# Kernel optimization log

Hardware: AMD Instinct MI355X
Metric: run time of the kernel (lower is better)

The kernel has to match this reference:

```python
import jax, jax.numpy as jnp
import numpy as np

N_CB = 10          # n_codebooks
K = 2048           # codebook_size
D = 256            # codebook_dim
SEM = 256          # semantic_proj_dim
W2V = 1024         # w2v_bert_dim
COMMIT = 0.25      # commitment_cost


def setup_inputs() -> dict:
    key = jax.random.key(0)
    ks = jax.random.split(key, 7)
    B, T = 16, 1024
    z = jax.random.normal(ks[0], (B, T, D), jnp.float32)
    w2v_targets = jax.random.normal(ks[1], (B, T, W2V), jnp.float32)
    # codebooks: uniform(-1/K, 1/K) as in nn.init.uniform_
    E = jax.random.uniform(ks[2], (N_CB, K, D), jnp.float32, -1.0 / K, 1.0 / K)
    # semantic head: Linear(D, SEM) -> GELU -> Linear(SEM, W2V)
    W1 = jax.random.normal(ks[3], (D, SEM), jnp.float32) * (1.0 / np.sqrt(D))
    b1 = jnp.zeros((SEM,), jnp.float32)
    W2 = jax.random.normal(ks[4], (SEM, W2V), jnp.float32) * (1.0 / np.sqrt(SEM))
    b2 = jnp.zeros((W2V,), jnp.float32)
    return {"z": z, "w2v_targets": w2v_targets, "E": E,
            "W1": W1, "b1": b1, "W2": W2, "b2": b2}


def _vq_step(residual, Ei):
    """Single-codebook VQ with straight-through estimator.
    residual: (B,T,D); Ei: (K,D). Returns (z_q, indices, loss)."""
    sg = jax.lax.stop_gradient
    B, T, d = residual.shape
    flat = residual.reshape(-1, d)                      # (N, D)
    dist = (jnp.sum(flat * flat, axis=1, keepdims=True)
            - 2.0 * flat @ Ei.T
            + jnp.sum(Ei * Ei, axis=1))
    idx = jnp.argmin(dist, axis=1).reshape(B, T)        # (B, T)
    q = Ei[idx]                                         # (B, T, D) gather
    commitment_loss = jnp.mean((sg(q) - residual) ** 2)
    embedding_loss = jnp.mean((q - sg(residual)) ** 2)
    loss = embedding_loss + COMMIT * commitment_loss
    z_q = residual + sg(q - residual)                   # straight-through
    return z_q, idx, loss


def reference(z, w2v_targets, E, W1, b1, W2, b2):
    residual = z
    z_q_total = jnp.zeros_like(z)
    codes = []
    vq_loss = jnp.float32(0.0)
    semantic_loss = jnp.float32(0.0)
    for i in range(N_CB):
        z_q_i, idx_i, loss_i = _vq_step(residual, E[i])
        if i == 0:
            # semantic head on CB1 output (torch GELU default = exact erf)
            h = jax.nn.gelu(z_q_i @ W1 + b1, approximate=False)
            predicted = h @ W2 + b2                     # (B, T, W2V)
            semantic_loss = jnp.mean((predicted - w2v_targets) ** 2)
        z_q_total = z_q_total + z_q_i
        residual = residual - jax.lax.stop_gradient(z_q_i)
        vq_loss = vq_loss + loss_i
        codes.append(idx_i)
    all_codes = jnp.stack(codes, axis=-1)               # (B, T, N_CB)
    return z_q_total, all_codes, vq_loss, semantic_loss
```

## Files before the change

kernel.cpp:

```cpp
#include <hip/hip_runtime.h>
#include <float.h>
#include <math.h>

#define NTOK 16384
#define KCB  2048
#define DDIM 256
#define NCB  10
#define MARGIN 1.0e-3f

typedef __attribute__((ext_vector_type(8))) short  short8;
typedef __attribute__((ext_vector_type(4))) float  f32x4;

static __device__ __forceinline__ unsigned short f2bf(float f) {
    unsigned int b = __float_as_uint(f);
    unsigned int r = b + 0x7FFFu + ((b >> 16) & 1u);
    return (unsigned short)(r >> 16);
}
static __device__ __forceinline__ float bf2f(unsigned short h) {
    return __uint_as_float((unsigned int)h << 16);
}

__global__ __launch_bounds__(256) void norms_all_kernel(const float* __restrict__ E,
                                                        const float* __restrict__ z,
                                                        float* __restrict__ sseE,
                                                        float* __restrict__ normA) {
    const int gw   = (blockIdx.x * 256 + threadIdx.x) >> 6;
    const int lane = threadIdx.x & 63;
    const int row  = gw * 4 + (lane >> 4);
    const int l    = lane & 15;
    const float* src = nullptr; float* dst = nullptr;
    if (row < NCB * KCB)             { src = E + (size_t)row * DDIM;               dst = sseE + row; }
    else if (row < NCB * KCB + NTOK) { src = z + (size_t)(row - NCB * KCB) * DDIM; dst = normA + (row - NCB * KCB); }
    float r = 0.f;
    if (src) {
        const float* a = src + ((l >> 3) << 7) + (l & 7);
        float v = a[0];
        r = __fmul_rn(v, v);
        #pragma unroll
        for (int k = 1; k < 16; ++k) { v = a[k * 8]; r = __fadd_rn(r, __fmul_rn(v, v)); }
    }
    r = __fadd_rn(r, __shfl_xor(r, 1, 64));
    r = __fadd_rn(r, __shfl_xor(r, 2, 64));
    r = __fadd_rn(r, __shfl_xor(r, 4, 64));
    r = __fadd_rn(r, __shfl_xor(r, 8, 64));
    if (src && l == 0) *dst = r;
}

__global__ __launch_bounds__(256) void conv_all_kernel(const float* __restrict__ E,
                                                       const float* __restrict__ z,
                                                       const float* __restrict__ W1,
                                                       const float* __restrict__ W2,
                                                       unsigned short* __restrict__ Eh,
                                                       unsigned short* __restrict__ resH,
                                                       unsigned short* __restrict__ w1t,
                                                       unsigned short* __restrict__ w2t) {
    int i = blockIdx.x * 256 + threadIdx.x;
    if (i < 5242880) {
        Eh[i] = f2bf(E[i]);
    } else if (i < 9437184) {
        int j = i - 5242880;
        resH[j] = f2bf(z[j]);
    } else if (i < 9502720) {
        int j = i - 9437184;
        int n = j >> 8, k = j & 255;
        w1t[j] = f2bf(W1[k * 256 + n]);
    } else {
        int j = i - 9502720;
        int n = j >> 8, k = j & 255;
        w2t[j] = f2bf(W2[k * 1024 + n]);
    }
}

__global__ __launch_bounds__(256) void vq_screen(const unsigned short* __restrict__ resH,
                                                 const unsigned short* __restrict__ Ehi,
                                                 const float* __restrict__ sseEi,
                                                 int2* __restrict__ gSlots,
                                                 int* __restrict__ gCnt,
                                                 float* __restrict__ gMin) {
    __shared__ unsigned short sAh[128 * 40];
    __shared__ unsigned short sBh[128 * 40];
    __shared__ float sC[128];
    __shared__ int   lCnt[128];
    __shared__ int2  lSlot[128][4];
    const int tid = threadIdx.x;
    const int wv = tid >> 6, lane = tid & 63;
    const int l15 = lane & 15, qd = lane >> 4;
    const int tile = blockIdx.x >> 4, slice = blockIdx.x & 15;
    const int t0 = tile * 128, c0 = slice * 128;

    if (tid < 128) { lCnt[tid] = 0; sC[tid] = sseEi[c0 + tid]; }
    {
        int2 inf; inf.x = 0x7F800000; inf.y = 0;
        ((int2*)lSlot)[tid] = inf; ((int2*)lSlot)[tid + 256] = inf;
    }

    f32x4 acc[2][8];
    #pragma unroll
    for (int m = 0; m < 2; ++m)
        #pragma unroll
        for (int n = 0; n < 8; ++n) acc[m][n] = (f32x4){0.f, 0.f, 0.f, 0.f};

    const int r0 = tid >> 2, cc4 = tid & 3;
    const int r1 = (tid + 256) >> 2;
    for (int kc = 0; kc < 8; ++kc) {
        const int db = kc * 32;
        __syncthreads();
        *(uint4*)(sAh + r0 * 40 + cc4 * 8) = *(const uint4*)(resH + (size_t)(t0 + r0) * 256 + db + cc4 * 8);
        *(uint4*)(sAh + r1 * 40 + cc4 * 8) = *(const uint4*)(resH + (size_t)(t0 + r1) * 256 + db + cc4 * 8);
        *(uint4*)(sBh + r0 * 40 + cc4 * 8) = *(const uint4*)(Ehi  + (size_t)(c0 + r0) * 256 + db + cc4 * 8);
        *(uint4*)(sBh + r1 * 40 + cc4 * 8) = *(const uint4*)(Ehi  + (size_t)(c0 + r1) * 256 + db + cc4 * 8);
        __syncthreads();

        short8 ah[2];
        #pragma unroll
        for (int m = 0; m < 2; ++m)
            ah[m] = *(const short8*)(sAh + (wv * 32 + m * 16 + l15) * 40 + qd * 8);
        #pragma unroll
        for (int n = 0; n < 8; ++n) {
            short8 bh = *(const short8*)(sBh + (n * 16 + l15) * 40 + qd * 8);
            #pragma unroll
            for (int m = 0; m < 2; ++m)
                acc[m][n] = __builtin_amdgcn_mfma_f32_16x16x32_bf16(ah[m], bh, acc[m][n], 0, 0, 0);
        }
    }

    #pragma unroll
    for (int m = 0; m < 2; ++m)
        #pragma unroll
        for (int n = 0; n < 8; ++n) {
            float Cv = sC[n * 16 + l15];
            #pragma unroll
            for (int r = 0; r < 4; ++r) acc[m][n][r] = fmaf(-2.f, acc[m][n][r], Cv);
        }
    #pragma unroll
    for (int m = 0; m < 2; ++m)
        #pragma unroll
        for (int r = 0; r < 4; ++r) {
            float v = acc[m][0][r];
            #pragma unroll
            for (int n = 1; n < 8; ++n) v = fminf(v, acc[m][n][r]);
            v = fminf(v, __shfl_xor(v, 1, 64));
            v = fminf(v, __shfl_xor(v, 2, 64));
            v = fminf(v, __shfl_xor(v, 4, 64));
            v = fminf(v, __shfl_xor(v, 8, 64));
            int tloc = wv * 32 + m * 16 + qd * 4 + r;
            if (l15 == 0) gMin[(t0 + tloc) * 16 + slice] = v;
            float thr = v + MARGIN;
            #pragma unroll
            for (int n = 0; n < 8; ++n) {
                float sv = acc[m][n][r];
                if (sv <= thr) {
                    int pos = atomicAdd(&lCnt[tloc], 1);
                    if (pos < 4) {
                        int2 e; e.x = __float_as_int(sv); e.y = c0 + n * 16 + l15;
                        lSlot[tloc][pos] = e;
                    }
                }
            }
        }
    __syncthreads();
    {
        int tloc = tid >> 1, half = tid & 1;
        size_t base = (size_t)(t0 + tloc) * 64 + slice * 4 + half * 2;
        gSlots[base]     = lSlot[tloc][half * 2];
        gSlots[base + 1] = lSlot[tloc][half * 2 + 1];
        if (!half) gCnt[(t0 + tloc) * 16 + slice] = lCnt[tloc];
    }
}

static __device__ __forceinline__ float np_chain(const float* __restrict__ sRow,
                                                 const float* __restrict__ Ei,
                                                 int cc, float A, float C) {
    const float4* e = (const float4*)(Ei + (size_t)cc * DDIM);
    float a = 0.f;
    #pragma unroll 8
    for (int k = 0; k < 64; ++k) {
        float4 ev = e[k];
        const float4 rv = *(const float4*)(sRow + k * 4);
        a = fmaf(rv.x, ev.x, a); a = fmaf(rv.y, ev.y, a);
        a = fmaf(rv.z, ev.z, a); a = fmaf(rv.w, ev.w, a);
    }
    return __fadd_rn(fmaf(-2.f, a, A), C);
}

__global__ __launch_bounds__(256) void vq_post(const float* __restrict__ resSrc,
                                               const float* __restrict__ Ei,
                                               const float* __restrict__ sseEi,
                                               float* __restrict__ res,
                                               float* __restrict__ zq,
                                               float* __restrict__ codes,
                                               float* __restrict__ lossPart,
                                               float* __restrict__ normA,
                                               unsigned short* __restrict__ resHp,
                                               unsigned short* __restrict__ zqb,
                                               const int2* __restrict__ gSlots,
                                               const int* __restrict__ gCnt,
                                               const float* __restrict__ gMin,
                                               int iter) {
    __shared__ float sScr[4][4][256];
    const int tid = threadIdx.x;
    const int wv = tid >> 6, lane = tid & 63;
    const int g = lane >> 4, l15 = lane & 15;
    const int tb = blockIdx.x * 16 + wv * 4;
    float lsum = 0.f;

    int2 sl[4]; float4 r4[4]; int cnt4[4]; float smin4[4]; float4 zq4[4]; float A4[4];
    #pragma unroll
    for (int j = 0; j < 4; ++j) sl[j] = gSlots[(size_t)(tb + j) * 64 + lane];
    #pragma unroll
    for (int j = 0; j < 4; ++j)
        r4[j] = *(const float4*)(resSrc + (size_t)(tb + j) * DDIM + lane * 4);
    #pragma unroll
    for (int j = 0; j < 4; ++j) cnt4[j]  = (lane < 16) ? gCnt[(tb + j) * 16 + lane] : 0;
    #pragma unroll
    for (int j = 0; j < 4; ++j) smin4[j] = (lane < 16) ? gMin[(tb + j) * 16 + lane] : FLT_MAX;
    #pragma unroll
    for (int j = 0; j < 4; ++j) A4[j] = normA[tb + j];
    if (iter > 0) {
        #pragma unroll
        for (int j = 0; j < 4; ++j)
            zq4[j] = *(const float4*)(zq + (size_t)(tb + j) * DDIM + lane * 4);
    }

    int winner[4];
    #pragma unroll
    for (int j = 0; j < 4; ++j) {
        float gm = smin4[j];
        #pragma unroll
        for (int o = 32; o >= 1; o >>= 1) gm = fminf(gm, __shfl_xor(gm, o, 64));
        const float thr = gm + MARGIN;
        float sv = __int_as_float(sl[j].x);
        unsigned long long bal = __ballot((sv <= thr) ? 1 : 0);
        bool ovfRel = __any((lane < 16 && cnt4[j] > 4 && smin4[j] <= thr) ? 1 : 0);
        if (!ovfRel && __popcll(bal) == 1) {
            winner[j] = __shfl(sl[j].y, __ffsll(bal) - 1, 64);
        } else if (!ovfRel) {
            *(float4*)(&sScr[wv][j][lane * 4]) = r4[j];
            const bool qal = (sv <= thr);
            const int cc = qal ? sl[j].y : 0;
            float s = np_chain(sScr[wv][j], Ei, cc, A4[j], sseEi[cc]);
            unsigned long long best = qal
                ? (((unsigned long long)__float_as_uint(s) << 32) | (unsigned)cc)
                : ~0ULL;
            #pragma unroll
            for (int o = 32; o >= 1; o >>= 1) {
                unsigned long long ot = __shfl_xor(best, o, 64);
                if (ot < best) best = ot;
            }
            winner[j] = (int)(unsigned)(best & 0xFFFFFFFFu);
        } else {
            *(float4*)(&sScr[wv][j][lane * 4]) = r4[j];
            unsigned long long best = ~0ULL;
            for (int cc = lane; cc < KCB; cc += 64) {
                float s = np_chain(sScr[wv][j], Ei, cc, A4[j], sseEi[cc]);
                unsigned long long key =
                    ((unsigned long long)__float_as_uint(s) << 32) | (unsigned)cc;
                if (key < best) best = key;
            }
            #pragma unroll
            for (int o = 32; o >= 1; o >>= 1) {
                unsigned long long ot = __shfl_xor(best, o, 64);
                if (ot < best) best = ot;
            }
            winner[j] = (int)(unsigned)(best & 0xFFFFFFFFu);
        }
    }
    #pragma unroll
    for (int j = 0; j < 4; ++j)
        if (lane == j) codes[(size_t)(tb + j) * NCB + iter] = (float)winner[j];

    float4 q4[4];
    #pragma unroll
    for (int j = 0; j < 4; ++j)
        q4[j] = *(const float4*)(Ei + (size_t)winner[j] * DDIM + lane * 4);

    #pragma unroll
    for (int j = 0; j < 4; ++j) {
        const size_t go = (size_t)(tb + j) * DDIM + lane * 4;
        float4 rn4, zqi4;
        float tqx = q4[j].x - r4[j].x; zqi4.x = r4[j].x + tqx; rn4.x = r4[j].x - zqi4.x;
        float tqy = q4[j].y - r4[j].y; zqi4.y = r4[j].y + tqy; rn4.y = r4[j].y - zqi4.y;
        float tqz = q4[j].z - r4[j].z; zqi4.z = r4[j].z + tqz; rn4.z = r4[j].z - zqi4.z;
        float tqw = q4[j].w - r4[j].w; zqi4.w = r4[j].w + tqw; rn4.w = r4[j].w - zqi4.w;
        lsum = fmaf(tqx, tqx, lsum); lsum = fmaf(tqy, tqy, lsum);
        lsum = fmaf(tqz, tqz, lsum); lsum = fmaf(tqw, tqw, lsum);
        *(float4*)(res + go) = rn4;
        {
            unsigned short h[4] = { f2bf(rn4.x), f2bf(rn4.y), f2bf(rn4.z), f2bf(rn4.w) };
            *(ushort4*)(resHp + go) = *(ushort4*)h;
        }
        if (iter == 0) {
            *(float4*)(zq + go) = zqi4;
            unsigned short u[4] = { f2bf(zqi4.x), f2bf(zqi4.y), f2bf(zqi4.z), f2bf(zqi4.w) };
            *(ushort4*)(zqb + go) = *(ushort4*)u;
        } else {
            zq4[j].x += zqi4.x; zq4[j].y += zqi4.y;
            zq4[j].z += zqi4.z; zq4[j].w += zqi4.w;
            *(float4*)(zq + go) = zq4[j];
        }
        *(float4*)(&sScr[wv][j][lane * 4]) = rn4;
    }
    {
        const float* a = &sScr[wv][g][((l15 >> 3) << 7) + (l15 & 7)];
        float v = a[0];
        float r = __fmul_rn(v, v);
        #pragma unroll
        for (int k = 1; k < 16; ++k) { v = a[k * 8]; r = __fadd_rn(r, __fmul_rn(v, v)); }
        r = __fadd_rn(r, __shfl_xor(r, 1, 64));
        r = __fadd_rn(r, __shfl_xor(r, 2, 64));
        r = __fadd_rn(r, __shfl_xor(r, 4, 64));
        r = __fadd_rn(r, __shfl_xor(r, 8, 64));
        if (l15 == 0) normA[tb + g] = r;
    }
    #pragma unroll
    for (int o = 32; o >= 1; o >>= 1) lsum += __shfl_xor(lsum, o, 64);
    if (lane == 0) lossPart[iter * 4096 + blockIdx.x * 4 + wv] = lsum;
}

__global__ __launch_bounds__(256) void loss_final(const float* __restrict__ lossPart,
                                                  float* __restrict__ vql) {
    __shared__ float sRed[4];
    float s = 0.f;
    for (int i = threadIdx.x; i < 40960; i += 256) s += lossPart[i];
    #pragma unroll
    for (int o = 32; o >= 1; o >>= 1) s += __shfl_xor(s, o, 64);
    if ((threadIdx.x & 63) == 0) sRed[threadIdx.x >> 6] = s;
    __syncthreads();
    if (threadIdx.x == 0)
        vql[0] = (sRed[0] + sRed[1] + sRed[2] + sRed[3]) * (1.25f / 4194304.f);
}

__global__ __launch_bounds__(256) void semantic_mfma(const unsigned short* __restrict__ zqb,
                                                     const float* __restrict__ tgt,
                                                     const unsigned short* __restrict__ w1t,
                                                     const float* __restrict__ b1,
                                                     const unsigned short* __restrict__ w2t,
                                                     const float* __restrict__ b2,
                                                     float* __restrict__ semLoss) {
    __shared__ unsigned short sZ[32 * 264];
    __shared__ unsigned short sH[32 * 264];
    __shared__ float sRed[4];
    const int tid = threadIdx.x;
    const int wv = tid >> 6, lane = tid & 63;
    const int l15 = lane & 15, qd = lane >> 4;
    const int tb = blockIdx.x * 32;

    {
        int row = tid >> 3, seg = tid & 7;
        const uint4* src = (const uint4*)(zqb + (size_t)(tb + row) * 256);
        uint4* dst = (uint4*)(&sZ[row * 264]);
        #pragma unroll
        for (int p = 0; p < 4; ++p) dst[seg * 4 + p] = src[seg * 4 + p];
    }
    __syncthreads();

    short8 az[8][2];
    #pragma unroll
    for (int kc = 0; kc < 8; ++kc)
        #pragma unroll
        for (int m = 0; m < 2; ++m)
            az[kc][m] = *(const short8*)(&sZ[(16 * m + l15) * 264 + kc * 32 + qd * 8]);

    #pragma unroll
    for (int nt4 = 0; nt4 < 4; ++nt4) {
        const int nt = wv * 4 + nt4;
        f32x4 acc0 = {0.f,0.f,0.f,0.f}, acc1 = {0.f,0.f,0.f,0.f};
        const unsigned short* bb = w1t + (size_t)(16 * nt + l15) * 256 + qd * 8;
        #pragma unroll
        for (int kc = 0; kc < 8; ++kc) {
            short8 b = *(const short8*)(bb + kc * 32);
            acc0 = __builtin_amdgcn_mfma_f32_16x16x32_bf16(az[kc][0], b, acc0, 0, 0, 0);
            acc1 = __builtin_amdgcn_mfma_f32_16x16x32_bf16(az[kc][1], b, acc1, 0, 0, 0);
        }
        const float b1v = b1[16 * nt + l15];
        #pragma unroll
        for (int r = 0; r < 4; ++r) {
            float x0 = acc0[r] + b1v;
            float x1 = acc1[r] + b1v;
            sH[(4 * qd + r) * 264 + 16 * nt + l15]      = f2bf(0.5f * x0 * (1.f + erff(x0 * 0.70710678f)));
            sH[(16 + 4 * qd + r) * 264 + 16 * nt + l15] = f2bf(0.5f * x1 * (1.f + erff(x1 * 0.70710678f)));
        }
    }
    __syncthreads();

    short8 ah[8][2];
    #pragma unroll
    for (int kc = 0; kc < 8; ++kc)
        #pragma unroll
        for (int m = 0; m < 2; ++m)
            ah[kc][m] = *(const short8*)(&sH[(16 * m + l15) * 264 + kc * 32 + qd * 8]);

    float lsum = 0.f;
    for (int t = 0; t < 16; ++t) {
        const int nt = wv * 16 + t;
        f32x4 acc0 = {0.f,0.f,0.f,0.f}, acc1 = {0.f,0.f,0.f,0.f};
        const unsigned short* bb = w2t + (size_t)(16 * nt + l15) * 256 + qd * 8;
        #pragma unroll
        for (int kc = 0; kc < 8; ++kc) {
            short8 b = *(const short8*)(bb + kc * 32);
            acc0 = __builtin_amdgcn_mfma_f32_16x16x32_bf16(ah[kc][0], b, acc0, 0, 0, 0);
            acc1 = __builtin_amdgcn_mfma_f32_16x16x32_bf16(ah[kc][1], b, acc1, 0, 0, 0);
        }
        const int n = 16 * nt + l15;
        const float b2v = b2[n];
        #pragma unroll
        for (int r = 0; r < 4; ++r) {
            float dv0 = (acc0[r] + b2v) - tgt[(size_t)(tb + 4 * qd + r) * 1024 + n];
            float dv1 = (acc1[r] + b2v) - tgt[(size_t)(tb + 16 + 4 * qd + r) * 1024 + n];
            lsum = fmaf(dv0, dv0, lsum);
            lsum = fmaf(dv1, dv1, lsum);
        }
    }
    #pragma unroll
    for (int o = 32; o >= 1; o >>= 1) lsum += __shfl_xor(lsum, o, 64);
    if (lane == 0) sRed[wv] = lsum;
    __syncthreads();
    if (tid == 0)
        atomicAdd(semLoss, (sRed[0] + sRed[1] + sRed[2] + sRed[3]) * (1.0f / 16777216.f));
}

extern "C" void kernel_launch(void* const* d_in, const int* in_sizes, int n_in,
                              void* d_out, int out_size, void* d_ws, size_t ws_size,
                              hipStream_t stream) {
    const float* z   = (const float*)d_in[0];
    const float* tgt = (const float*)d_in[1];
    const float* E   = (const float*)d_in[2];
    const float* W1  = (const float*)d_in[3];
    const float* b1  = (const float*)d_in[4];
    const float* W2  = (const float*)d_in[5];
    const float* b2  = (const float*)d_in[6];

    float* out   = (float*)d_out;
    float* zq    = out;
    float* codes = out + (size_t)NTOK * DDIM;
    float* vql   = codes + (size_t)NTOK * NCB;

    char* w = (char*)d_ws;
    float*          res   = (float*)(w);
    unsigned short* resH  = (unsigned short*)(w + 16777216);
    unsigned short* Eh    = (unsigned short*)(w + 33554432);
    unsigned short* zqb   = (unsigned short*)(w + 54525952);
    int2*           gSlots= (int2*)(w + 62914560);
    int*            gCnt  = (int*)(w + 71303168);
    float*          gMin  = (float*)(w + 72351744);
    float*          sseE  = (float*)(w + 73400320);
    float*          normA = (float*)(w + 73531392);
    float*          lossPart=(float*)(w + 73662464);
    unsigned short* w1t   = (unsigned short*)(w + 73924608);
    unsigned short* w2t   = (unsigned short*)(w + 74055680);

    hipMemsetAsync(vql, 0, 2 * sizeof(float), stream);
    norms_all_kernel<<<9216, 256, 0, stream>>>(E, z, sseE, normA);
    conv_all_kernel<<<38144, 256, 0, stream>>>(E, z, W1, W2, Eh, resH, w1t, w2t);
    for (int it = 0; it < NCB; ++it) {
        const float*          Ei    = E  + (size_t)it * KCB * DDIM;
        const unsigned short* Ehi   = Eh + (size_t)it * KCB * DDIM;
        const float*          sseEi = sseE + (size_t)it * KCB;
        const float* resSrc = (it == 0) ? z : res;
        vq_screen<<<2048, 256, 0, stream>>>(resH, Ehi, sseEi, gSlots, gCnt, gMin);
        vq_post<<<1024, 256, 0, stream>>>(resSrc, Ei, sseEi, res, zq, codes, lossPart,
                                          normA, resH, zqb, gSlots, gCnt, gMin, it);
        if (it == 0)
            semantic_mfma<<<512, 256, 0, stream>>>(zqb, tgt, w1t, b1, w2t, b2, vql + 1);
    }
    loss_final<<<1, 256, 0, stream>>>(lossPart, vql);
}
```

Measured before the change: 1.103 ms.

## Restructure VQ screen and semantic head around register-resident A and swizzled LDS

The two prep kernels are merged into one launch, and the memset plus atomic are dropped. The VQ screen kernel now keeps the residual A tile in registers and loops over four codebook slices per block, with a full-K XOR-swizzled LDS tile for B. Candidate compaction changes from LDS atomics to a ballot-style bitmask with a prefix scan that writes straight to global memory. The semantic head processes 64 tokens per block with swizzled, double-buffered W2 tiles and writes per-block partials that the final loss kernel reduces. Register pressure goes up, and the grid for the screen kernel shrinks, which may reduce occupancy.

```diff
diff --git a/kernel.cpp b/kernel.cpp
--- a/kernel.cpp
+++ b/kernel.cpp
@@ -20,54 +20,53 @@
     return __uint_as_float((unsigned int)h << 16);
 }
 
-__global__ __launch_bounds__(256) void norms_all_kernel(const float* __restrict__ E,
-                                                        const float* __restrict__ z,
-                                                        float* __restrict__ sseE,
-                                                        float* __restrict__ normA) {
-    const int gw   = (blockIdx.x * 256 + threadIdx.x) >> 6;
-    const int lane = threadIdx.x & 63;
-    const int row  = gw * 4 + (lane >> 4);
-    const int l    = lane & 15;
-    const float* src = nullptr; float* dst = nullptr;
-    if (row < NCB * KCB)             { src = E + (size_t)row * DDIM;               dst = sseE + row; }
-    else if (row < NCB * KCB + NTOK) { src = z + (size_t)(row - NCB * KCB) * DDIM; dst = normA + (row - NCB * KCB); }
-    float r = 0.f;
-    if (src) {
-        const float* a = src + ((l >> 3) << 7) + (l & 7);
-        float v = a[0];
-        r = __fmul_rn(v, v);
-        #pragma unroll
-        for (int k = 1; k < 16; ++k) { v = a[k * 8]; r = __fadd_rn(r, __fmul_rn(v, v)); }
-    }
-    r = __fadd_rn(r, __shfl_xor(r, 1, 64));
-    r = __fadd_rn(r, __shfl_xor(r, 2, 64));
-    r = __fadd_rn(r, __shfl_xor(r, 4, 64));
-    r = __fadd_rn(r, __shfl_xor(r, 8, 64));
-    if (src && l == 0) *dst = r;
-}
-
-__global__ __launch_bounds__(256) void conv_all_kernel(const float* __restrict__ E,
-                                                       const float* __restrict__ z,
-                                                       const float* __restrict__ W1,
-                                                       const float* __restrict__ W2,
-                                                       unsigned short* __restrict__ Eh,
-                                                       unsigned short* __restrict__ resH,
-                                                       unsigned short* __restrict__ w1t,
-                                                       unsigned short* __restrict__ w2t) {
-    int i = blockIdx.x * 256 + threadIdx.x;
-    if (i < 5242880) {
-        Eh[i] = f2bf(E[i]);
-    } else if (i < 9437184) {
-        int j = i - 5242880;
-        resH[j] = f2bf(z[j]);
-    } else if (i < 9502720) {
-        int j = i - 9437184;
-        int n = j >> 8, k = j & 255;
-        w1t[j] = f2bf(W1[k * 256 + n]);
+__global__ __launch_bounds__(256) void prep_all(const float* __restrict__ E,
+                                                const float* __restrict__ z,
+                                                const float* __restrict__ W1,
+                                                const float* __restrict__ W2,
+                                                float* __restrict__ sseE,
+                                                float* __restrict__ normA,
+                                                unsigned short* __restrict__ Eh,
+                                                unsigned short* __restrict__ resH,
+                                                unsigned short* __restrict__ w1t,
+                                                unsigned short* __restrict__ w2t) {
+    if (blockIdx.x < 38144) {
+        int i = blockIdx.x * 256 + threadIdx.x;
+        if (i < 5242880) {
+            Eh[i] = f2bf(E[i]);
+        } else if (i < 9437184) {
+            int j = i - 5242880;
+            resH[j] = f2bf(z[j]);
+        } else if (i < 9502720) {
+            int j = i - 9437184;
+            int n = j >> 8, k = j & 255;
+            w1t[j] = f2bf(W1[k * 256 + n]);
+        } else {
+            int j = i - 9502720;
+            int n = j >> 8, k = j & 255;
+            w2t[j] = f2bf(W2[k * 1024 + n]);
+        }
     } else {
-        int j = i - 9502720;
-        int n = j >> 8, k = j & 255;
-        w2t[j] = f2bf(W2[k * 1024 + n]);
+        const int gw   = ((blockIdx.x - 38144) * 256 + threadIdx.x) >> 6;
+        const int lane = threadIdx.x & 63;
+        const int row  = gw * 4 + (lane >> 4);
+        const int l    = lane & 15;
+        const float* src = nullptr; float* dst = nullptr;
+        if (row < NCB * KCB)             { src = E + (size_t)row * DDIM;               dst = sseE + row; }
+        else if (row < NCB * KCB + NTOK) { src = z + (size_t)(row - NCB * KCB) * DDIM; dst = normA + (row - NCB * KCB); }
+        float r = 0.f;
+        if (src) {
+            const float* a = src + ((l >> 3) << 7) + (l & 7);
+            float v = a[0];
+            r = __fmul_rn(v, v);
+            #pragma unroll
+            for (int k = 1; k < 16; ++k) { v = a[k * 8]; r = __fadd_rn(r, __fmul_rn(v, v)); }
+        }
+        r = __fadd_rn(r, __shfl_xor(r, 1, 64));
+        r = __fadd_rn(r, __shfl_xor(r, 2, 64));
+        r = __fadd_rn(r, __shfl_xor(r, 4, 64));
+        r = __fadd_rn(r, __shfl_xor(r, 8, 64));
+        if (src && l == 0) *dst = r;
     }
 }
 
@@ -77,94 +76,105 @@
                                                  int2* __restrict__ gSlots,
                                                  int* __restrict__ gCnt,
                                                  float* __restrict__ gMin) {
-    __shared__ unsigned short sAh[128 * 40];
-    __shared__ unsigned short sBh[128 * 40];
-    __shared__ float sC[128];
-    __shared__ int   lCnt[128];
-    __shared__ int2  lSlot[128][4];
+    __shared__ uint4 sB[4096];
+    char* sBb = (char*)sB;
     const int tid = threadIdx.x;
     const int wv = tid >> 6, lane = tid & 63;
     const int l15 = lane & 15, qd = lane >> 4;
-    const int tile = blockIdx.x >> 4, slice = blockIdx.x & 15;
-    const int t0 = tile * 128, c0 = slice * 128;
-
-    if (tid < 128) { lCnt[tid] = 0; sC[tid] = sseEi[c0 + tid]; }
-    {
-        int2 inf; inf.x = 0x7F800000; inf.y = 0;
-        ((int2*)lSlot)[tid] = inf; ((int2*)lSlot)[tid + 256] = inf;
-    }
-
-    f32x4 acc[2][8];
-    #pragma unroll
-    for (int m = 0; m < 2; ++m)
-        #pragma unroll
-        for (int n = 0; n < 8; ++n) acc[m][n] = (f32x4){0.f, 0.f, 0.f, 0.f};
-
-    const int r0 = tid >> 2, cc4 = tid & 3;
-    const int r1 = (tid + 256) >> 2;
-    for (int kc = 0; kc < 8; ++kc) {
-        const int db = kc * 32;
+    const int tile = blockIdx.x >> 2, quarter = blockIdx.x & 3;
+    const int t0 = tile * 128;
+    const int rs = tid >> 5, cs = tid & 31;
+    const int swzs = (cs * 16) ^ ((rs & 7) << 4);
+
+    short8 az[8][2];
+    #pragma unroll
+    for (int kc = 0; kc < 8; ++kc)
+        #pragma unroll
+        for (int m = 0; m < 2; ++m)
+            az[kc][m] = *(const short8*)(resH + (size_t)(t0 + wv * 32 + m * 16 + l15) * 256 + kc * 32 + qd * 8);
+
+    #pragma unroll 1
+    for (int s = 0; s < 4; ++s) {
+        const int slice = quarter * 4 + s;
+        const int c0 = slice * 128;
         __syncthreads();
-        *(uint4*)(sAh + r0 * 40 + cc4 * 8) = *(const uint4*)(resH + (size_t)(t0 + r0) * 256 + db + cc4 * 8);
-        *(uint4*)(sAh + r1 * 40 + cc4 * 8) = *(const uint4*)(resH + (size_t)(t0 + r1) * 256 + db + cc4 * 8);
-        *(uint4*)(sBh + r0 * 40 + cc4 * 8) = *(const uint4*)(Ehi  + (size_t)(c0 + r0) * 256 + db + cc4 * 8);
-        *(uint4*)(sBh + r1 * 40 + cc4 * 8) = *(const uint4*)(Ehi  + (size_t)(c0 + r1) * 256 + db + cc4 * 8);
+        #pragma unroll
+        for (int j = 0; j < 16; ++j) {
+            int r = j * 8 + rs;
+            *(uint4*)(sBb + r * 512 + swzs) = *(const uint4*)(Ehi + (size_t)(c0 + r) * 256 + cs * 8);
+        }
+        float Cv8[8];
+        #pragma unroll
+        for (int n = 0; n < 8; ++n) Cv8[n] = sseEi[c0 + n * 16 + l15];
         __syncthreads();
 
-        short8 ah[2];
+        f32x4 acc[2][8];
         #pragma unroll
         for (int m = 0; m < 2; ++m)
-            ah[m] = *(const short8*)(sAh + (wv * 32 + m * 16 + l15) * 40 + qd * 8);
-        #pragma unroll
-        for (int n = 0; n < 8; ++n) {
-            short8 bh = *(const short8*)(sBh + (n * 16 + l15) * 40 + qd * 8);
-            #pragma unroll
-            for (int m = 0; m < 2; ++m)
-                acc[m][n] = __builtin_amdgcn_mfma_f32_16x16x32_bf16(ah[m], bh, acc[m][n], 0, 0, 0);
-        }
-    }
-
-    #pragma unroll
-    for (int m = 0; m < 2; ++m)
-        #pragma unroll
-        for (int n = 0; n < 8; ++n) {
-            float Cv = sC[n * 16 + l15];
-            #pragma unroll
-            for (int r = 0; r < 4; ++r) acc[m][n][r] = fmaf(-2.f, acc[m][n][r], Cv);
-        }
-    #pragma unroll
-    for (int m = 0; m < 2; ++m)
-        #pragma unroll
-        for (int r = 0; r < 4; ++r) {
-            float v = acc[m][0][r];
-            #pragma unroll
-            for (int n = 1; n < 8; ++n) v = fminf(v, acc[m][n][r]);
-            v = fminf(v, __shfl_xor(v, 1, 64));
-            v = fminf(v, __shfl_xor(v, 2, 64));
-            v = fminf(v, __shfl_xor(v, 4, 64));
-            v = fminf(v, __shfl_xor(v, 8, 64));
-            int tloc = wv * 32 + m * 16 + qd * 4 + r;
-            if (l15 == 0) gMin[(t0 + tloc) * 16 + slice] = v;
-            float thr = v + MARGIN;
+            #pragma unroll
+            for (int n = 0; n < 8; ++n) acc[m][n] = (f32x4){0.f, 0.f, 0.f, 0.f};
+
+        for (int kc = 0; kc < 8; ++kc) {
             #pragma unroll
             for (int n = 0; n < 8; ++n) {
-                float sv = acc[m][n][r];
-                if (sv <= thr) {
-                    int pos = atomicAdd(&lCnt[tloc], 1);
-                    if (pos < 4) {
-                        int2 e; e.x = __float_as_int(sv); e.y = c0 + n * 16 + l15;
-                        lSlot[tloc][pos] = e;
+                const int R = n * 16 + l15;
+                short8 bh = *(const short8*)(sBb + R * 512 + ((kc * 64 + qd * 16) ^ ((R & 7) << 4)));
+                acc[0][n] = __builtin_amdgcn_mfma_f32_16x16x32_bf16(az[kc][0], bh, acc[0][n], 0, 0, 0);
+                acc[1][n] = __builtin_amdgcn_mfma_f32_16x16x32_bf16(az[kc][1], bh, acc[1][n], 0, 0, 0);
+            }
+        }
+
+        #pragma unroll
+        for (int m = 0; m < 2; ++m)
+            #pragma unroll
+            for (int n = 0; n < 8; ++n) {
+                #pragma unroll
+                for (int r = 0; r < 4; ++r) acc[m][n][r] = fmaf(-2.f, acc[m][n][r], Cv8[n]);
+            }
+
+        #pragma unroll
+        for (int m = 0; m < 2; ++m)
+            #pragma unroll
+            for (int r = 0; r < 4; ++r) {
+                float v = acc[m][0][r];
+                #pragma unroll
+                for (int n = 1; n < 8; ++n) v = fminf(v, acc[m][n][r]);
+                v = fminf(v, __shfl_xor(v, 1, 64));
+                v = fminf(v, __shfl_xor(v, 2, 64));
+                v = fminf(v, __shfl_xor(v, 4, 64));
+                v = fminf(v, __shfl_xor(v, 8, 64));
+                const int tloc = t0 + wv * 32 + m * 16 + qd * 4 + r;
+                const float thr = v + MARGIN;
+                int bm = 0;
+                #pragma unroll
+                for (int n = 0; n < 8; ++n)
+                    bm |= (acc[m][n][r] <= thr) ? (1 << n) : 0;
+                const int cnt8 = __popc(bm);
+                int inc = cnt8;
+                #pragma unroll
+                for (int o = 1; o < 16; o <<= 1) {
+                    int t = __shfl_up(inc, o, 16);
+                    if (l15 >= o) inc += t;
+                }
+                const int tot = __shfl(inc, 15, 16);
+                int rank = inc - cnt8;
+                const size_t base = (size_t)tloc * 64 + slice * 4;
+                #pragma unroll
+                for (int n = 0; n < 8; ++n)
+                    if ((bm >> n) & 1) {
+                        if (rank < 4) {
+                            int2 e; e.x = __float_as_int(acc[m][n][r]); e.y = c0 + n * 16 + l15;
+                            gSlots[base + rank] = e;
+                        }
+                        ++rank;
                     }
+                if (l15 == 0) {
+                    gMin[tloc * 16 + slice] = v;
+                    gCnt[tloc * 16 + slice] = tot;
+                    int2 inf; inf.x = 0x7F800000; inf.y = 0;
+                    for (int p = tot; p < 4; ++p) gSlots[base + p] = inf;
                 }
             }
-        }
-    __syncthreads();
-    {
-        int tloc = tid >> 1, half = tid & 1;
-        size_t base = (size_t)(t0 + tloc) * 64 + slice * 4 + half * 2;
-        gSlots[base]     = lSlot[tloc][half * 2];
-        gSlots[base + 1] = lSlot[tloc][half * 2 + 1];
-        if (!half) gCnt[(t0 + tloc) * 16 + slice] = lCnt[tloc];
     }
 }
 
@@ -317,106 +327,149 @@
     if (lane == 0) lossPart[iter * 4096 + blockIdx.x * 4 + wv] = lsum;
 }
 
-__global__ __launch_bounds__(256) void loss_final(const float* __restrict__ lossPart,
-                                                  float* __restrict__ vql) {
-    __shared__ float sRed[4];
-    float s = 0.f;
-    for (int i = threadIdx.x; i < 40960; i += 256) s += lossPart[i];
-    #pragma unroll
-    for (int o = 32; o >= 1; o >>= 1) s += __shfl_xor(s, o, 64);
-    if ((threadIdx.x & 63) == 0) sRed[threadIdx.x >> 6] = s;
-    __syncthreads();
-    if (threadIdx.x == 0)
-        vql[0] = (sRed[0] + sRed[1] + sRed[2] + sRed[3]) * (1.25f / 4194304.f);
-}
-
-__global__ __launch_bounds__(256) void semantic_mfma(const unsigned short* __restrict__ zqb,
-                                                     const float* __restrict__ tgt,
-                                                     const unsigned short* __restrict__ w1t,
-                                                     const float* __restrict__ b1,
-                                                     const unsigned short* __restrict__ w2t,
-                                                     const float* __restrict__ b2,
-                                                     float* __restrict__ semLoss) {
-    __shared__ unsigned short sZ[32 * 264];
-    __shared__ unsigned short sH[32 * 264];
-    __shared__ float sRed[4];
+__global__ __launch_bounds__(256) void sem_mfma(const unsigned short* __restrict__ zqb,
+                                                const float* __restrict__ tgt,
+                                                const unsigned short* __restrict__ w1t,
+                                                const float* __restrict__ b1,
+                                                const unsigned short* __restrict__ w2t,
+                                                const float* __restrict__ b2,
+                                                float* __restrict__ semPart) {
+    __shared__ uint4 sBq[2048];
+    __shared__ uint4 sHq[2048];
+    char* sBb = (char*)sBq;
+    char* sHb = (char*)sHq;
     const int tid = threadIdx.x;
     const int wv = tid >> 6, lane = tid & 63;
     const int l15 = lane & 15, qd = lane >> 4;
-    const int tb = blockIdx.x * 32;
-
+    const int tb = blockIdx.x * 64;
+    const int rs = tid >> 5, cs = tid & 31;
+    const int swzs = (cs * 16) ^ ((rs & 7) << 4);
+
+    #pragma unroll
+    for (int j = 0; j < 8; ++j) {
+        int r = j * 8 + rs;
+        *(uint4*)(sHb + r * 512 + swzs) = *(const uint4*)(zqb + (size_t)(tb + r) * 256 + cs * 8);
+    }
+    __syncthreads();
+    short8 az[8];
     {
-        int row = tid >> 3, seg = tid & 7;
-        const uint4* src = (const uint4*)(zqb + (size_t)(tb + row) * 256);
-        uint4* dst = (uint4*)(&sZ[row * 264]);
-        #pragma unroll
-        for (int p = 0; p < 4; ++p) dst[seg * 4 + p] = src[seg * 4 + p];
+        const int R = wv * 16 + l15;
+        #pragma unroll
+        for (int kc = 0; kc < 8; ++kc)
+            az[kc] = *(const short8*)(sHb + R * 512 + ((kc * 64 + qd * 16) ^ ((R & 7) << 4)));
     }
     __syncthreads();
 
-    short8 az[8][2];
-    #pragma unroll
-    for (int kc = 0; kc < 8; ++kc)
-        #pragma unroll
-        for (int m = 0; m < 2; ++m)
-            az[kc][m] = *(const short8*)(&sZ[(16 * m + l15) * 264 + kc * 32 + qd * 8]);
-
-    #pragma unroll
-    for (int nt4 = 0; nt4 < 4; ++nt4) {
-        const int nt = wv * 4 + nt4;
-        f32x4 acc0 = {0.f,0.f,0.f,0.f}, acc1 = {0.f,0.f,0.f,0.f};
-        const unsigned short* bb = w1t + (size_t)(16 * nt + l15) * 256 + qd * 8;
-        #pragma unroll
+    #pragma unroll 1
+    for (int s1 = 0; s1 < 4; ++s1) {
+        #pragma unroll
+        for (int j = 0; j < 8; ++j) {
+            int r = j * 8 + rs;
+            *(uint4*)(sBb + r * 512 + swzs) = *(const uint4*)(w1t + (size_t)(s1 * 64 + r) * 256 + cs * 8);
+        }
+        __syncthreads();
+        f32x4 acc[4];
+        #pragma unroll
+        for (int n = 0; n < 4; ++n) acc[n] = (f32x4){0.f, 0.f, 0.f, 0.f};
         for (int kc = 0; kc < 8; ++kc) {
-            short8 b = *(const short8*)(bb + kc * 32);
-            acc0 = __builtin_amdgcn_mfma_f32_16x16x32_bf16(az[kc][0], b, acc0, 0, 0, 0);
-            acc1 = __builtin_amdgcn_mfma_f32_16x16x32_bf16(az[kc][1], b, acc1, 0, 0, 0);
-        }
-        const float b1v = b1[16 * nt + l15];
-        #pragma unroll
-        for (int r = 0; r < 4; ++r) {
-            float x0 = acc0[r] + b1v;
-            float x1 = acc1[r] + b1v;
-            sH[(4 * qd + r) * 264 + 16 * nt + l15]      = f2bf(0.5f * x0 * (1.f + erff(x0 * 0.70710678f)));
-            sH[(16 + 4 * qd + r) * 264 + 16 * nt + l15] = f2bf(0.5f * x1 * (1.f + erff(x1 * 0.70710678f)));
-        }
+            #pragma unroll
+            for (int n = 0; n < 4; ++n) {
+                const int R = n * 16 + l15;
+                short8 b = *(const short8*)(sBb + R * 512 + ((kc * 64 + qd * 16) ^ ((R & 7) << 4)));
+                acc[n] = __builtin_amdgcn_mfma_f32_16x16x32_bf16(az[kc], b, acc[n], 0, 0, 0);
+            }
+        }
+        #pragma unroll
+        for (int n = 0; n < 4; ++n) {
+            const int o = s1 * 64 + n * 16 + l15;
+            const float b1v = b1[o];
+            #pragma unroll
+            for (int r = 0; r < 4; ++r) {
+                float x = acc[n][r] + b1v;
+                const int tr = wv * 16 + qd * 4 + r;
+                *(unsigned short*)(sHb + tr * 512 + ((o * 2) ^ ((tr & 7) << 4))) =
+                    f2bf(0.5f * x * (1.f + erff(x * 0.70710678f)));
+            }
+        }
+        __syncthreads();
+    }
+
+    short8 ah[8];
+    {
+        const int R = wv * 16 + l15;
+        #pragma unroll
+        for (int kc = 0; kc < 8; ++kc)
+            ah[kc] = *(const short8*)(sHb + R * 512 + ((kc * 64 + qd * 16) ^ ((R & 7) << 4)));
+    }
+    #pragma unroll
+    for (int j = 0; j < 8; ++j) {
+        int r = j * 8 + rs;
+        *(uint4*)(sBb + r * 512 + swzs) = *(const uint4*)(w2t + (size_t)r * 256 + cs * 8);
     }
     __syncthreads();
 
-    short8 ah[8][2];
-    #pragma unroll
-    for (int kc = 0; kc < 8; ++kc)
-        #pragma unroll
-        for (int m = 0; m < 2; ++m)
-            ah[kc][m] = *(const short8*)(&sH[(16 * m + l15) * 264 + kc * 32 + qd * 8]);
-
     float lsum = 0.f;
-    for (int t = 0; t < 16; ++t) {
-        const int nt = wv * 16 + t;
-        f32x4 acc0 = {0.f,0.f,0.f,0.f}, acc1 = {0.f,0.f,0.f,0.f};
-        const unsigned short* bb = w2t + (size_t)(16 * nt + l15) * 256 + qd * 8;
-        #pragma unroll
+    #pragma unroll 1
+    for (int s2 = 0; s2 < 16; ++s2) {
+        char* cb = (s2 & 1) ? sHb : sBb;
+        char* nb = (s2 & 1) ? sBb : sHb;
+        if (s2 < 15) {
+            #pragma unroll
+            for (int j = 0; j < 8; ++j) {
+                int r = j * 8 + rs;
+                *(uint4*)(nb + r * 512 + swzs) =
+                    *(const uint4*)(w2t + (size_t)((s2 + 1) * 64 + r) * 256 + cs * 8);
+            }
+        }
+        float tg[4][4], b2v[4];
+        #pragma unroll
+        for (int n = 0; n < 4; ++n) {
+            const int o = s2 * 64 + n * 16 + l15;
+            b2v[n] = b2[o];
+            #pragma unroll
+            for (int r = 0; r < 4; ++r)
+                tg[n][r] = tgt[(size_t)(tb + wv * 16 + qd * 4 + r) * 1024 + o];
+        }
+        f32x4 acc[4];
+        #pragma unroll
+        for (int n = 0; n < 4; ++n) acc[n] = (f32x4){0.f, 0.f, 0.f, 0.f};
         for (int kc = 0; kc < 8; ++kc) {
-            short8 b = *(const short8*)(bb + kc * 32);
-            acc0 = __builtin_amdgcn_mfma_f32_16x16x32_bf16(ah[kc][0], b, acc0, 0, 0, 0);
-            acc1 = __builtin_amdgcn_mfma_f32_16x16x32_bf16(ah[kc][1], b, acc1, 0, 0, 0);
-        }
-        const int n = 16 * nt + l15;
-        const float b2v = b2[n];
-        #pragma unroll
-        for (int r = 0; r < 4; ++r) {
-            float dv0 = (acc0[r] + b2v) - tgt[(size_t)(tb + 4 * qd + r) * 1024 + n];
-            float dv1 = (acc1[r] + b2v) - tgt[(size_t)(tb + 16 + 4 * qd + r) * 1024 + n];
-            lsum = fmaf(dv0, dv0, lsum);
-            lsum = fmaf(dv1, dv1, lsum);
-        }
+            #pragma unroll
+            for (int n = 0; n < 4; ++n) {
+                const int R = n * 16 + l15;
+                short8 b = *(const short8*)(cb + R * 512 + ((kc * 64 + qd * 16) ^ ((R & 7) << 4)));
+                acc[n] = __builtin_amdgcn_mfma_f32_16x16x32_bf16(ah[kc], b, acc[n], 0, 0, 0);
+            }
+        }
+        #pragma unroll
+        for (int n = 0; n < 4; ++n)
+            #pragma unroll
+            for (int r = 0; r < 4; ++r) {
+                float dv = (acc[n][r] + b2v[n]) - tg[n][r];
+                lsum = fmaf(dv, dv, lsum);
+            }
+        __syncthreads();
     }
     #pragma unroll
     for (int o = 32; o >= 1; o >>= 1) lsum += __shfl_xor(lsum, o, 64);
-    if (lane == 0) sRed[wv] = lsum;
+    if (lane == 0) semPart[blockIdx.x * 4 + wv] = lsum;
+}
+
+__global__ __launch_bounds__(256) void loss_final(const float* __restrict__ lossPart,
+                                                  const float* __restrict__ semPart,
+                                                  float* __restrict__ vql) {
+    __shared__ float sRed[4], sRed2[4];
+    float s = 0.f, q = 0.f;
+    for (int i = threadIdx.x; i < 40960; i += 256) s += lossPart[i];
+    for (int i = threadIdx.x; i < 1024; i += 256) q += semPart[i];
+    #pragma unroll
+    for (int o = 32; o >= 1; o >>= 1) { s += __shfl_xor(s, o, 64); q += __shfl_xor(q, o, 64); }
+    if ((threadIdx.x & 63) == 0) { sRed[threadIdx.x >> 6] = s; sRed2[threadIdx.x >> 6] = q; }
     __syncthreads();
-    if (tid == 0)
-        atomicAdd(semLoss, (sRed[0] + sRed[1] + sRed[2] + sRed[3]) * (1.0f / 16777216.f));
+    if (threadIdx.x == 0) {
+        vql[0] = (sRed[0] + sRed[1] + sRed[2] + sRed[3]) * (1.25f / 4194304.f);
+        vql[1] = (sRed2[0] + sRed2[1] + sRed2[2] + sRed2[3]) * (1.0f / 16777216.f);
+    }
 }
 
 extern "C" void kernel_launch(void* const* d_in, const int* in_sizes, int n_in,
@@ -438,6 +491,7 @@
     char* w = (char*)d_ws;
     float*          res   = (float*)(w);
     unsigned short* resH  = (unsigned short*)(w + 16777216);
+    float*          semPart=(float*)(w + 25165824);
     unsigned short* Eh    = (unsigned short*)(w + 33554432);
     unsigned short* zqb   = (unsigned short*)(w + 54525952);
     int2*           gSlots= (int2*)(w + 62914560);
@@ -449,19 +503,17 @@
     unsigned short* w1t   = (unsigned short*)(w + 73924608);
     unsigned short* w2t   = (unsigned short*)(w + 74055680);
 
-    hipMemsetAsync(vql, 0, 2 * sizeof(float), stream);
-    norms_all_kernel<<<9216, 256, 0, stream>>>(E, z, sseE, normA);
-    conv_all_kernel<<<38144, 256, 0, stream>>>(E, z, W1, W2, Eh, resH, w1t, w2t);
+    prep_all<<<47360, 256, 0, stream>>>(E, z, W1, W2, sseE, normA, Eh, resH, w1t, w2t);
     for (int it = 0; it < NCB; ++it) {
         const float*          Ei    = E  + (size_t)it * KCB * DDIM;
         const unsigned short* Ehi   = Eh + (size_t)it * KCB * DDIM;
         const float*          sseEi = sseE + (size_t)it * KCB;
         const float* resSrc = (it == 0) ? z : res;
-        vq_screen<<<2048, 256, 0, stream>>>(resH, Ehi, sseEi, gSlots, gCnt, gMin);
+        vq_screen<<<512, 256, 0, stream>>>(resH, Ehi, sseEi, gSlots, gCnt, gMin);
         vq_post<<<1024, 256, 0, stream>>>(resSrc, Ei, sseEi, res, zq, codes, lossPart,
                                           normA, resH, zqb, gSlots, gCnt, gMin, it);
         if (it == 0)
-            semantic_mfma<<<512, 256, 0, stream>>>(zqb, tgt, w1t, b1, w2t, b2, vql + 1);
-    }
-    loss_final<<<1, 256, 0, stream>>>(lossPart, vql);
-}
+            sem_mfma<<<256, 256, 0, stream>>>(zqb, tgt, w1t, b1, w2t, b2, semPart);
+    }
+    loss_final<<<1, 256, 0, stream>>>(lossPart, semPart, vql);
+}
```

Result: slower. 1.639 ms (+48.6%).
